# Performance work log

Measured on AMD Instinct MI355X. Metric: run time of the kernel, lower is better.

## Reference

```python
import jax, jax.numpy as jnp
import numpy as np

BN_EPS = 1e-5


def adder_conv(x, w, stride=1):
    """AdderNet L1-distance 'convolution': out = -sum_k |patch_k - w_k|.
    x: [B, Cin, H, W], w: [Cout, Cin, kh, kw] -> [B, Cout, Ho, Wo]."""
    Cout, Cin, kh, kw = w.shape
    # patches: [B, Cin*kh*kw, Ho, Wo], feature order (cin, kh, kw)
    patches = jax.lax.conv_general_dilated_patches(
        x, (kh, kw), (stride, stride), 'VALID')
    wf = w.reshape(Cout, Cin * kh * kw)
    # [B,1,K,Ho,Wo] - [1,Cout,K,1,1] -> reduce over K
    return -jnp.abs(patches[:, None] - wf[None, :, :, None, None]).sum(axis=2)


def batchnorm(x, gamma, beta):
    # training-mode BN (batch statistics, biased variance) as torch does in forward
    m = x.mean(axis=(0, 2, 3), keepdims=True)
    v = x.var(axis=(0, 2, 3), keepdims=True)
    xn = (x - m) * jax.lax.rsqrt(v + BN_EPS)
    return xn * gamma.reshape(1, -1, 1, 1) + beta.reshape(1, -1, 1, 1)


def maxpool(x, k):
    return jax.lax.reduce_window(x, -jnp.inf, jax.lax.max,
                                 (1, 1, k, k), (1, 1, k, k), 'VALID')


def setup_inputs() -> dict:
    key = jax.random.key(0)
    ks = jax.random.split(key, 4)
    B = 64
    inputs = jax.random.normal(ks[0], (B, 1, 499, 12), dtype=jnp.float32)
    w1 = jax.random.normal(ks[1], (5, 1, 12, 5), dtype=jnp.float32) * 0.1
    w2 = jax.random.normal(ks[2], (10, 5, 5, 1), dtype=jnp.float32) * 0.1
    w_fc = jax.random.normal(ks[3], (10, 590, 1, 1), dtype=jnp.float32) * 0.05
    return {
        'inputs': inputs,
        'w1': w1, 'g1': jnp.ones(5, jnp.float32), 'b1': jnp.zeros(5, jnp.float32),
        'w2': w2, 'g2': jnp.ones(10, jnp.float32), 'b2': jnp.zeros(10, jnp.float32),
        'w_fc': w_fc, 'g3': jnp.ones(10, jnp.float32), 'b3': jnp.zeros(10, jnp.float32),
    }


def reference(inputs, w1, g1, b1, w2, g2, b2, w_fc, g3, b3):
    x = adder_conv(inputs, w1)                 # [B,5,488,8]
    x = jax.nn.relu(batchnorm(x, g1, b1))
    x = maxpool(x, 4)                          # [B,5,122,2]
    x = adder_conv(x, w2)                      # [B,10,118,2]
    x = jax.nn.relu(batchnorm(x, g2, b2))
    x = maxpool(x, 2)                          # [B,10,59,1]
    B = x.shape[0]
    x = x.reshape(B, -1, 1, 1)                 # [B,590,1,1]
    x = adder_conv(x, w_fc)                    # [B,10,1,1]
    x = batchnorm(x, g3, b3)
    return x.reshape(B, -1)                    # [B,10]
```

## Files before the change

### kernel.cpp

```cpp
#include <hip/hip_runtime.h>


#define BN_EPS 1e-5f

__global__ void zero_stats_kernel(double* stats) {
    if (threadIdx.x < 64) stats[threadIdx.x] = 0.0;
}

__global__ __launch_bounds__(256) void conv1p1_kernel(
    const float* __restrict__ in, const float* __restrict__ w1,
    float* __restrict__ Bo, double* __restrict__ stats)
{
    int bid = blockIdx.x;
    int t  = bid & 1;
    int bc = bid >> 1;
    int co = bc % 5;
    int b  = bc / 5;
    int tid = threadIdx.x;

    __shared__ float img[255 * 12 + 4];
    const float4* ip4 = (const float4*)(in + b * 5988 + t * 2928);
    float4* img4 = (float4*)img;
    for (int i = tid; i < 765; i += 256) img4[i] = ip4[i];

    float w[60];
    #pragma unroll
    for (int i = 0; i < 60; i++) w[i] = w1[co * 60 + i];
    __syncthreads();

    float ls = 0.f, lss = 0.f;
    float m0 = 0.f, m1 = 0.f;
    if (tid < 244) {
        int y = tid;
        float s[8] = {0.f,0.f,0.f,0.f,0.f,0.f,0.f,0.f};
        #pragma unroll
        for (int kh = 0; kh < 12; kh++) {
            const float* rp = &img[(y + kh) * 12];
            float4 r0 = *(const float4*)(rp);
            float4 r1 = *(const float4*)(rp + 4);
            float4 r2 = *(const float4*)(rp + 8);
            float row[12] = {r0.x,r0.y,r0.z,r0.w, r1.x,r1.y,r1.z,r1.w, r2.x,r2.y,r2.z,r2.w};
            #pragma unroll
            for (int x = 0; x < 8; x++) {
                #pragma unroll
                for (int kw = 0; kw < 5; kw++)
                    s[x] += fabsf(row[x + kw] - w[kh * 5 + kw]);
            }
        }
        float o[8];
        #pragma unroll
        for (int x = 0; x < 8; x++) { o[x] = -s[x]; ls += o[x]; lss += o[x] * o[x]; }
        m0 = fmaxf(fmaxf(o[0], o[1]), fmaxf(o[2], o[3]));
        m1 = fmaxf(fmaxf(o[4], o[5]), fmaxf(o[6], o[7]));
    }
    m0 = fmaxf(m0, __shfl_down(m0, 1, 64));
    m0 = fmaxf(m0, __shfl_down(m0, 2, 64));
    m1 = fmaxf(m1, __shfl_down(m1, 1, 64));
    m1 = fmaxf(m1, __shfl_down(m1, 2, 64));
    if (tid < 244 && (tid & 3) == 0) {
        int p = t * 61 + (tid >> 2);
        float* bp = Bo + ((size_t)(b * 5 + co) * 122 + p) * 2;
        bp[0] = m0; bp[1] = m1;
    }

    __shared__ double rs[256], rss[256];
    rs[tid] = (double)ls; rss[tid] = (double)lss;
    __syncthreads();
    for (int ofs = 128; ofs > 0; ofs >>= 1) {
        if (tid < ofs) { rs[tid] += rs[tid + ofs]; rss[tid] += rss[tid + ofs]; }
        __syncthreads();
    }
    if (tid == 0) {
        atomicAdd(&stats[co],     rs[0]);
        atomicAdd(&stats[8 + co], rss[0]);
    }
}

__global__ __launch_bounds__(64) void conv2p2_kernel(
    const float* __restrict__ Bi, double* __restrict__ stats,
    const float* __restrict__ g1, const float* __restrict__ b1,
    const float* __restrict__ w2,
    float* __restrict__ Draw)
{
    int bid = blockIdx.x;
    int co = bid % 10;
    int b  = bid / 10;
    int tid = threadIdx.x;

    float sc1[5], sh1[5];
    const double N1 = 64.0 * 488.0 * 8.0;
    #pragma unroll
    for (int c = 0; c < 5; c++) {
        double m = stats[c] / N1;
        double v = stats[8 + c] / N1 - m * m;
        sc1[c] = g1[c] * rsqrtf((float)v + BN_EPS);
        sh1[c] = b1[c] - (float)m * sc1[c];
    }

    __shared__ float img[5 * 122 * 2];
    const float4* bp4 = (const float4*)(Bi + (size_t)b * 1220);
    float4* img4 = (float4*)img;
    for (int i = tid; i < 305; i += 64) {
        int c = i / 61;
        float4 r = bp4[i];
        r.x = fmaxf(0.f, r.x * sc1[c] + sh1[c]);
        r.y = fmaxf(0.f, r.y * sc1[c] + sh1[c]);
        r.z = fmaxf(0.f, r.z * sc1[c] + sh1[c]);
        r.w = fmaxf(0.f, r.w * sc1[c] + sh1[c]);
        img4[i] = r;
    }

    float w[25];
    #pragma unroll
    for (int i = 0; i < 25; i++) w[i] = w2[co * 25 + i];
    __syncthreads();

    float ls = 0.f, lss = 0.f;
    if (tid < 59) {
        const float2* img2 = (const float2*)img;
        float o[4];
        #pragma unroll
        for (int r = 0; r < 2; r++) {
            int row = 2 * tid + r;
            float s0 = 0.f, s1 = 0.f;
            #pragma unroll
            for (int cin = 0; cin < 5; cin++)
                #pragma unroll
                for (int kh = 0; kh < 5; kh++) {
                    float2 f = img2[cin * 122 + row + kh];
                    float wv = w[cin * 5 + kh];
                    s0 += fabsf(f.x - wv);
                    s1 += fabsf(f.y - wv);
                }
            o[r * 2]     = -s0;
            o[r * 2 + 1] = -s1;
        }
        #pragma unroll
        for (int i = 0; i < 4; i++) { ls += o[i]; lss += o[i] * o[i]; }
        Draw[(size_t)(b * 10 + co) * 59 + tid] =
            fmaxf(fmaxf(o[0], o[1]), fmaxf(o[2], o[3]));
    }

    #pragma unroll
    for (int ofs = 32; ofs > 0; ofs >>= 1) {
        ls  += __shfl_down(ls, ofs, 64);
        lss += __shfl_down(lss, ofs, 64);
    }
    if (tid == 0) {
        atomicAdd(&stats[16 + co], (double)ls);
        atomicAdd(&stats[32 + co], (double)lss);
    }
}

__global__ __launch_bounds__(256) void fc_kernel(
    const float* __restrict__ Draw, const double* __restrict__ stats,
    const float* __restrict__ g2, const float* __restrict__ b2,
    const float* __restrict__ wfc, float* __restrict__ E)
{
    int tid = threadIdx.x;
    __shared__ float sc2[10], sh2[10];
    if (tid < 10) {
        const double N2 = 64.0 * 118.0 * 2.0;
        double m = stats[16 + tid] / N2;
        double v = stats[32 + tid] / N2 - m * m;
        float sc = g2[tid] * rsqrtf((float)v + BN_EPS);
        sc2[tid] = sc;
        sh2[tid] = b2[tid] - (float)m * sc;
    }
    __syncthreads();

    int pair = blockIdx.x * 4 + (tid >> 6);
    int lane = tid & 63;
    int b = pair / 10, co = pair % 10;
    const float* dp = Draw + (size_t)b * 590;
    const float* wp = wfc + (size_t)co * 590;
    float s = 0.f;
    #pragma unroll
    for (int j = 0; j < 10; j++) {
        int k = lane + j * 64;
        if (k < 590) {
            int c = k / 59;
            float x = fmaxf(0.f, dp[k] * sc2[c] + sh2[c]);
            s += fabsf(x - wp[k]);
        }
    }
    #pragma unroll
    for (int ofs = 32; ofs > 0; ofs >>= 1) s += __shfl_down(s, ofs, 64);
    if (lane == 0) E[pair] = -s;
}

__global__ __launch_bounds__(640) void bn3_kernel(
    const float* __restrict__ E,
    const float* __restrict__ g3, const float* __restrict__ b3,
    float* __restrict__ out)
{
    int tid = threadIdx.x;
    int co = tid % 10;
    float o = E[tid];
    __shared__ float scale_s[10], shift_s[10];
    if (tid < 10) {
        double sm = 0.0, ss = 0.0;
        for (int bb = 0; bb < 64; bb++) {
            double v = (double)E[bb * 10 + tid];
            sm += v; ss += v * v;
        }
        double m = sm / 64.0;
        double v = ss / 64.0 - m * m;
        float sc = g3[tid] * rsqrtf((float)v + BN_EPS);
        scale_s[tid] = sc;
        shift_s[tid] = b3[tid] - (float)m * sc;
    }
    __syncthreads();
    out[tid] = o * scale_s[co] + shift_s[co];
}

extern "C" void kernel_launch(void* const* d_in, const int* in_sizes, int n_in,
                              void* d_out, int out_size, void* d_ws, size_t ws_size,
                              hipStream_t stream) {
    const float* in  = (const float*)d_in[0];
    const float* w1  = (const float*)d_in[1];
    const float* g1  = (const float*)d_in[2];
    const float* b1  = (const float*)d_in[3];
    const float* w2  = (const float*)d_in[4];
    const float* g2  = (const float*)d_in[5];
    const float* b2  = (const float*)d_in[6];
    const float* wfc = (const float*)d_in[7];
    const float* g3  = (const float*)d_in[8];
    const float* b3  = (const float*)d_in[9];
    float* out = (float*)d_out;

    double* stats = (double*)d_ws;
    float* Bv   = (float*)((char*)d_ws + 512);
    float* Draw = Bv + 78080;
    float* Ev   = Draw + 37760;

    zero_stats_kernel<<<1, 64, 0, stream>>>(stats);
    conv1p1_kernel<<<640, 256, 0, stream>>>(in, w1, Bv, stats);
    conv2p2_kernel<<<640, 64, 0, stream>>>(Bv, stats, g1, b1, w2, Draw);
    fc_kernel<<<160, 256, 0, stream>>>(Draw, stats, g2, b2, wfc, Ev);
    bn3_kernel<<<1, 640, 0, stream>>>(Ev, g3, b3, out);
}
```

Before: 106.4 us.

## Replace atomic BN stats with per-block partials, fuse FC and final BN

Each block now writes its BN partial sums to its own slot instead of doing double-precision atomics into shared counters. The consumer kernels reduce those partials with wave shuffles, which removes the zero-init kernel. The FC and the third batchnorm are merged into one 1024-thread single-block kernel that stages the FC weights in LDS. This cuts two kernel launches and the atomic contention, at the cost of running the FC stage on one workgroup.

```diff
diff --git a/kernel.cpp b/kernel.cpp
--- a/kernel.cpp
+++ b/kernel.cpp
@@ -2,14 +2,10 @@
 
 
 #define BN_EPS 1e-5f
-
-__global__ void zero_stats_kernel(double* stats) {
-    if (threadIdx.x < 64) stats[threadIdx.x] = 0.0;
-}
 
 __global__ __launch_bounds__(256) void conv1p1_kernel(
     const float* __restrict__ in, const float* __restrict__ w1,
-    float* __restrict__ Bo, double* __restrict__ stats)
+    float* __restrict__ Bo, double* __restrict__ p1)
 {
     int bid = blockIdx.x;
     int t  = bid & 1;
@@ -71,13 +67,14 @@
         __syncthreads();
     }
     if (tid == 0) {
-        atomicAdd(&stats[co],     rs[0]);
-        atomicAdd(&stats[8 + co], rss[0]);
+        p1[co * 128 + b * 2 + t]       = rs[0];
+        p1[640 + co * 128 + b * 2 + t] = rss[0];
     }
 }
 
 __global__ __launch_bounds__(64) void conv2p2_kernel(
-    const float* __restrict__ Bi, double* __restrict__ stats,
+    const float* __restrict__ Bi, const double* __restrict__ p1,
+    double* __restrict__ p2,
     const float* __restrict__ g1, const float* __restrict__ b1,
     const float* __restrict__ w2,
     float* __restrict__ Draw)
@@ -91,8 +88,17 @@
     const double N1 = 64.0 * 488.0 * 8.0;
     #pragma unroll
     for (int c = 0; c < 5; c++) {
-        double m = stats[c] / N1;
-        double v = stats[8 + c] / N1 - m * m;
+        double s = p1[c * 128 + tid] + p1[c * 128 + 64 + tid];
+        double q = p1[640 + c * 128 + tid] + p1[640 + c * 128 + 64 + tid];
+        #pragma unroll
+        for (int ofs = 32; ofs > 0; ofs >>= 1) {
+            s += __shfl_down(s, ofs, 64);
+            q += __shfl_down(q, ofs, 64);
+        }
+        s = __shfl(s, 0, 64);
+        q = __shfl(q, 0, 64);
+        double m = s / N1;
+        double v = q / N1 - m * m;
         sc1[c] = g1[c] * rsqrtf((float)v + BN_EPS);
         sh1[c] = b1[c] - (float)m * sc1[c];
     }
@@ -141,77 +147,105 @@
             fmaxf(fmaxf(o[0], o[1]), fmaxf(o[2], o[3]));
     }
 
+    double dls = (double)ls, dlss = (double)lss;
     #pragma unroll
     for (int ofs = 32; ofs > 0; ofs >>= 1) {
-        ls  += __shfl_down(ls, ofs, 64);
-        lss += __shfl_down(lss, ofs, 64);
+        dls  += __shfl_down(dls, ofs, 64);
+        dlss += __shfl_down(dlss, ofs, 64);
     }
     if (tid == 0) {
-        atomicAdd(&stats[16 + co], (double)ls);
-        atomicAdd(&stats[32 + co], (double)lss);
-    }
-}
-
-__global__ __launch_bounds__(256) void fc_kernel(
-    const float* __restrict__ Draw, const double* __restrict__ stats,
+        p2[co * 64 + b]       = dls;
+        p2[640 + co * 64 + b] = dlss;
+    }
+}
+
+__global__ __launch_bounds__(1024) void fcbn3_kernel(
+    const float* __restrict__ Draw, const double* __restrict__ p2,
     const float* __restrict__ g2, const float* __restrict__ b2,
-    const float* __restrict__ wfc, float* __restrict__ E)
-{
-    int tid = threadIdx.x;
-    __shared__ float sc2[10], sh2[10];
-    if (tid < 10) {
-        const double N2 = 64.0 * 118.0 * 2.0;
-        double m = stats[16 + tid] / N2;
-        double v = stats[32 + tid] / N2 - m * m;
-        float sc = g2[tid] * rsqrtf((float)v + BN_EPS);
-        sc2[tid] = sc;
-        sh2[tid] = b2[tid] - (float)m * sc;
-    }
-    __syncthreads();
-
-    int pair = blockIdx.x * 4 + (tid >> 6);
-    int lane = tid & 63;
-    int b = pair / 10, co = pair % 10;
-    const float* dp = Draw + (size_t)b * 590;
-    const float* wp = wfc + (size_t)co * 590;
-    float s = 0.f;
-    #pragma unroll
-    for (int j = 0; j < 10; j++) {
-        int k = lane + j * 64;
-        if (k < 590) {
-            int c = k / 59;
-            float x = fmaxf(0.f, dp[k] * sc2[c] + sh2[c]);
-            s += fabsf(x - wp[k]);
-        }
-    }
-    #pragma unroll
-    for (int ofs = 32; ofs > 0; ofs >>= 1) s += __shfl_down(s, ofs, 64);
-    if (lane == 0) E[pair] = -s;
-}
-
-__global__ __launch_bounds__(640) void bn3_kernel(
-    const float* __restrict__ E,
+    const float* __restrict__ wfc,
     const float* __restrict__ g3, const float* __restrict__ b3,
     float* __restrict__ out)
 {
-    int tid = threadIdx.x;
-    int co = tid % 10;
-    float o = E[tid];
-    __shared__ float scale_s[10], shift_s[10];
-    if (tid < 10) {
-        double sm = 0.0, ss = 0.0;
-        for (int bb = 0; bb < 64; bb++) {
-            double v = (double)E[bb * 10 + tid];
-            sm += v; ss += v * v;
-        }
-        double m = sm / 64.0;
-        double v = ss / 64.0 - m * m;
-        float sc = g3[tid] * rsqrtf((float)v + BN_EPS);
-        scale_s[tid] = sc;
-        shift_s[tid] = b3[tid] - (float)m * sc;
-    }
-    __syncthreads();
-    out[tid] = o * scale_s[co] + shift_s[co];
+    int tid  = threadIdx.x;
+    int w    = tid >> 6;
+    int lane = tid & 63;
+
+    __shared__ float wsm[5900];
+    __shared__ float E_lds[640];
+    __shared__ float sc2s[10], sh2s[10], sc3s[10], sh3s[10];
+
+    const float4* wf4 = (const float4*)wfc;
+    float4* wsm4 = (float4*)wsm;
+    for (int i = tid; i < 1475; i += 1024) wsm4[i] = wf4[i];
+
+    if (w < 10) {
+        const double N2 = 64.0 * 118.0 * 2.0;
+        double s = p2[w * 64 + lane];
+        double q = p2[640 + w * 64 + lane];
+        #pragma unroll
+        for (int ofs = 32; ofs > 0; ofs >>= 1) {
+            s += __shfl_down(s, ofs, 64);
+            q += __shfl_down(q, ofs, 64);
+        }
+        if (lane == 0) {
+            double m = s / N2;
+            double v = q / N2 - m * m;
+            float sc = g2[w] * rsqrtf((float)v + BN_EPS);
+            sc2s[w] = sc;
+            sh2s[w] = b2[w] - (float)m * sc;
+        }
+    }
+    __syncthreads();
+
+    for (int i = 0; i < 4; i++) {
+        int b = w * 4 + i;
+        float x[10];
+        #pragma unroll
+        for (int it = 0; it < 10; it++) {
+            int k = it * 64 + lane;
+            float xv = 0.f;
+            if (k < 590) {
+                int c = k / 59;
+                xv = fmaxf(0.f, Draw[b * 590 + k] * sc2s[c] + sh2s[c]);
+            }
+            x[it] = xv;
+        }
+        for (int co = 0; co < 10; co++) {
+            float s = 0.f;
+            #pragma unroll
+            for (int it = 0; it < 10; it++) {
+                int k = it * 64 + lane;
+                if (k < 590) s += fabsf(x[it] - wsm[co * 590 + k]);
+            }
+            #pragma unroll
+            for (int ofs = 32; ofs > 0; ofs >>= 1) s += __shfl_down(s, ofs, 64);
+            if (lane == 0) E_lds[b * 10 + co] = -s;
+        }
+    }
+    __syncthreads();
+
+    if (w < 10) {
+        float e = E_lds[lane * 10 + w];
+        double s = (double)e, q = (double)e * (double)e;
+        #pragma unroll
+        for (int ofs = 32; ofs > 0; ofs >>= 1) {
+            s += __shfl_down(s, ofs, 64);
+            q += __shfl_down(q, ofs, 64);
+        }
+        if (lane == 0) {
+            double m = s / 64.0;
+            double v = q / 64.0 - m * m;
+            float sc = g3[w] * rsqrtf((float)v + BN_EPS);
+            sc3s[w] = sc;
+            sh3s[w] = b3[w] - (float)m * sc;
+        }
+    }
+    __syncthreads();
+
+    if (tid < 640) {
+        int co = tid % 10;
+        out[tid] = E_lds[tid] * sc3s[co] + sh3s[co];
+    }
 }
 
 extern "C" void kernel_launch(void* const* d_in, const int* in_sizes, int n_in,
@@ -229,14 +263,12 @@
     const float* b3  = (const float*)d_in[9];
     float* out = (float*)d_out;
 
-    double* stats = (double*)d_ws;
-    float* Bv   = (float*)((char*)d_ws + 512);
+    double* p1 = (double*)d_ws;
+    double* p2 = p1 + 1280;
+    float* Bv   = (float*)((char*)d_ws + 20480);
     float* Draw = Bv + 78080;
-    float* Ev   = Draw + 37760;
-
-    zero_stats_kernel<<<1, 64, 0, stream>>>(stats);
-    conv1p1_kernel<<<640, 256, 0, stream>>>(in, w1, Bv, stats);
-    conv2p2_kernel<<<640, 64, 0, stream>>>(Bv, stats, g1, b1, w2, Draw);
-    fc_kernel<<<160, 256, 0, stream>>>(Draw, stats, g2, b2, wfc, Ev);
-    bn3_kernel<<<1, 640, 0, stream>>>(Ev, g3, b3, out);
-}
+
+    conv1p1_kernel<<<640, 256, 0, stream>>>(in, w1, Bv, p1);
+    conv2p2_kernel<<<640, 64, 0, stream>>>(Bv, p1, p2, g1, b1, w2, Draw);
+    fcbn3_kernel<<<1, 1024, 0, stream>>>(Draw, p2, g2, b2, wfc, g3, b3, out);
+}
```

Measured after the change: 110.9 us. +4.2%, slower.

## Replace stat atomics with per-block partials and fuse BN3 via last-block counter

Applied to the files above, without the earlier changes.

Global double atomicAdd statistics are replaced by per-block partial sums written to workspace. Consumers now reduce those partials themselves, which removes the zero-stats kernel. The final BN3 kernel is folded into the FC kernel: a counter makes the last block to finish compute the batch statistics and write the output. This cuts two launches and the atomic contention, at the cost of redundant partial reductions in every conv2 block and a threadfence/counter handshake.

```diff
diff --git a/kernel.cpp b/kernel.cpp
--- a/kernel.cpp
+++ b/kernel.cpp
@@ -2,16 +2,14 @@
 
 
 #define BN_EPS 1e-5f
-
-__global__ void zero_stats_kernel(double* stats) {
-    if (threadIdx.x < 64) stats[threadIdx.x] = 0.0;
-}
 
 __global__ __launch_bounds__(256) void conv1p1_kernel(
     const float* __restrict__ in, const float* __restrict__ w1,
-    float* __restrict__ Bo, double* __restrict__ stats)
+    float* __restrict__ Bo, double* __restrict__ p1,
+    unsigned int* __restrict__ counter)
 {
     int bid = blockIdx.x;
+    if (bid == 0 && threadIdx.x == 0) *counter = 0;
     int t  = bid & 1;
     int bc = bid >> 1;
     int co = bc % 5;
@@ -71,13 +69,14 @@
         __syncthreads();
     }
     if (tid == 0) {
-        atomicAdd(&stats[co],     rs[0]);
-        atomicAdd(&stats[8 + co], rss[0]);
+        p1[co * 128 + b * 2 + t]       = rs[0];
+        p1[640 + co * 128 + b * 2 + t] = rss[0];
     }
 }
 
 __global__ __launch_bounds__(64) void conv2p2_kernel(
-    const float* __restrict__ Bi, double* __restrict__ stats,
+    const float* __restrict__ Bi, const double* __restrict__ p1,
+    double* __restrict__ p2,
     const float* __restrict__ g1, const float* __restrict__ b1,
     const float* __restrict__ w2,
     float* __restrict__ Draw)
@@ -91,8 +90,17 @@
     const double N1 = 64.0 * 488.0 * 8.0;
     #pragma unroll
     for (int c = 0; c < 5; c++) {
-        double m = stats[c] / N1;
-        double v = stats[8 + c] / N1 - m * m;
+        double s = p1[c * 128 + tid] + p1[c * 128 + 64 + tid];
+        double q = p1[640 + c * 128 + tid] + p1[640 + c * 128 + 64 + tid];
+        #pragma unroll
+        for (int ofs = 32; ofs > 0; ofs >>= 1) {
+            s += __shfl_down(s, ofs, 64);
+            q += __shfl_down(q, ofs, 64);
+        }
+        s = __shfl(s, 0, 64);
+        q = __shfl(q, 0, 64);
+        double m = s / N1;
+        double v = q / N1 - m * m;
         sc1[c] = g1[c] * rsqrtf((float)v + BN_EPS);
         sh1[c] = b1[c] - (float)m * sc1[c];
     }
@@ -141,31 +149,41 @@
             fmaxf(fmaxf(o[0], o[1]), fmaxf(o[2], o[3]));
     }
 
+    double dls = (double)ls, dlss = (double)lss;
     #pragma unroll
     for (int ofs = 32; ofs > 0; ofs >>= 1) {
-        ls  += __shfl_down(ls, ofs, 64);
-        lss += __shfl_down(lss, ofs, 64);
+        dls  += __shfl_down(dls, ofs, 64);
+        dlss += __shfl_down(dlss, ofs, 64);
     }
     if (tid == 0) {
-        atomicAdd(&stats[16 + co], (double)ls);
-        atomicAdd(&stats[32 + co], (double)lss);
-    }
-}
-
-__global__ __launch_bounds__(256) void fc_kernel(
-    const float* __restrict__ Draw, const double* __restrict__ stats,
+        p2[co * 64 + b]       = dls;
+        p2[640 + co * 64 + b] = dlss;
+    }
+}
+
+__global__ __launch_bounds__(256) void fc_bn3_kernel(
+    const float* __restrict__ Draw, const double* __restrict__ p2,
     const float* __restrict__ g2, const float* __restrict__ b2,
-    const float* __restrict__ wfc, float* __restrict__ E)
+    const float* __restrict__ wfc,
+    const float* __restrict__ g3, const float* __restrict__ b3,
+    float* __restrict__ E, unsigned int* __restrict__ counter,
+    float* __restrict__ out)
 {
     int tid = threadIdx.x;
-    __shared__ float sc2[10], sh2[10];
+
+    __shared__ float sc2s[10], sh2s[10];
     if (tid < 10) {
         const double N2 = 64.0 * 118.0 * 2.0;
-        double m = stats[16 + tid] / N2;
-        double v = stats[32 + tid] / N2 - m * m;
+        double s = 0.0, q = 0.0;
+        for (int bb = 0; bb < 64; bb++) {
+            s += p2[tid * 64 + bb];
+            q += p2[640 + tid * 64 + bb];
+        }
+        double m = s / N2;
+        double v = q / N2 - m * m;
         float sc = g2[tid] * rsqrtf((float)v + BN_EPS);
-        sc2[tid] = sc;
-        sh2[tid] = b2[tid] - (float)m * sc;
+        sc2s[tid] = sc;
+        sh2s[tid] = b2[tid] - (float)m * sc;
     }
     __syncthreads();
 
@@ -180,38 +198,45 @@
         int k = lane + j * 64;
         if (k < 590) {
             int c = k / 59;
-            float x = fmaxf(0.f, dp[k] * sc2[c] + sh2[c]);
+            float x = fmaxf(0.f, dp[k] * sc2s[c] + sh2s[c]);
             s += fabsf(x - wp[k]);
         }
     }
     #pragma unroll
     for (int ofs = 32; ofs > 0; ofs >>= 1) s += __shfl_down(s, ofs, 64);
-    if (lane == 0) E[pair] = -s;
-}
-
-__global__ __launch_bounds__(640) void bn3_kernel(
-    const float* __restrict__ E,
-    const float* __restrict__ g3, const float* __restrict__ b3,
-    float* __restrict__ out)
-{
-    int tid = threadIdx.x;
-    int co = tid % 10;
-    float o = E[tid];
-    __shared__ float scale_s[10], shift_s[10];
-    if (tid < 10) {
-        double sm = 0.0, ss = 0.0;
-        for (int bb = 0; bb < 64; bb++) {
-            double v = (double)E[bb * 10 + tid];
-            sm += v; ss += v * v;
-        }
-        double m = sm / 64.0;
-        double v = ss / 64.0 - m * m;
-        float sc = g3[tid] * rsqrtf((float)v + BN_EPS);
-        scale_s[tid] = sc;
-        shift_s[tid] = b3[tid] - (float)m * sc;
-    }
-    __syncthreads();
-    out[tid] = o * scale_s[co] + shift_s[co];
+    if (lane == 0) atomicExch(&E[pair], -s);
+
+    __shared__ unsigned int lastflag;
+    __syncthreads();
+    if (tid == 0) {
+        __threadfence();
+        lastflag = (atomicAdd(counter, 1u) == 159u) ? 1u : 0u;
+    }
+    __syncthreads();
+    if (lastflag) {
+        __threadfence();
+        __shared__ float E_lds[640];
+        __shared__ float sc3s[10], sh3s[10];
+        for (int i = tid; i < 640; i += 256) E_lds[i] = E[i];
+        __syncthreads();
+        if (tid < 10) {
+            double sm = 0.0, ss = 0.0;
+            for (int bb = 0; bb < 64; bb++) {
+                double v = (double)E_lds[bb * 10 + tid];
+                sm += v; ss += v * v;
+            }
+            double m = sm / 64.0;
+            double v = ss / 64.0 - m * m;
+            float sc = g3[tid] * rsqrtf((float)v + BN_EPS);
+            sc3s[tid] = sc;
+            sh3s[tid] = b3[tid] - (float)m * sc;
+        }
+        __syncthreads();
+        for (int i = tid; i < 640; i += 256) {
+            int c = i % 10;
+            out[i] = E_lds[i] * sc3s[c] + sh3s[c];
+        }
+    }
 }
 
 extern "C" void kernel_launch(void* const* d_in, const int* in_sizes, int n_in,
@@ -229,14 +254,15 @@
     const float* b3  = (const float*)d_in[9];
     float* out = (float*)d_out;
 
-    double* stats = (double*)d_ws;
-    float* Bv   = (float*)((char*)d_ws + 512);
+    double* p1 = (double*)d_ws;
+    double* p2 = p1 + 1280;
+    float* Bv   = (float*)((char*)d_ws + 20480);
     float* Draw = Bv + 78080;
     float* Ev   = Draw + 37760;
-
-    zero_stats_kernel<<<1, 64, 0, stream>>>(stats);
-    conv1p1_kernel<<<640, 256, 0, stream>>>(in, w1, Bv, stats);
-    conv2p2_kernel<<<640, 64, 0, stream>>>(Bv, stats, g1, b1, w2, Draw);
-    fc_kernel<<<160, 256, 0, stream>>>(Draw, stats, g2, b2, wfc, Ev);
-    bn3_kernel<<<1, 640, 0, stream>>>(Ev, g3, b3, out);
-}
+    unsigned int* counter = (unsigned int*)(Ev + 640);
+
+    conv1p1_kernel<<<640, 256, 0, stream>>>(in, w1, Bv, p1, counter);
+    conv2p2_kernel<<<640, 64, 0, stream>>>(Bv, p1, p2, g1, b1, w2, Draw);
+    fc_bn3_kernel<<<160, 256, 0, stream>>>(Draw, p2, g2, b2, wfc, g3, b3,
+                                           Ev, counter, out);
+}
```

Result: faster. 97.99 us, median of 2 (-7.9%).
